# Kernel tuning notes

Hardware: AMD Instinct MI355X
Metric: run time of the kernel (lower is better)

Reference implementation:

```python
import jax, jax.numpy as jnp
import numpy as np

T = 20        # obs_len + pred_len
G = 1024      # number of scenes (groups)
P = 64        # pedestrians per scene (uniform groups)
THR = 0.25    # collision_threshold


def setup_inputs() -> dict:
    key = jax.random.key(0)
    k1, k2 = jax.random.split(key)
    trajectory = jax.random.normal(k1, (T, G * P, 2), dtype=jnp.float32)
    trajectory_relative = jax.random.normal(k2, (T, G * P, 2), dtype=jnp.float32)
    starts = jnp.arange(G, dtype=jnp.int32) * P
    seq_start_end = jnp.stack([starts, starts + P], axis=1)  # (G, 2)
    return {
        "trajectory": trajectory,
        "trajectory_relative": trajectory_relative,
        "seq_start_end": seq_start_end,
    }


def reference(trajectory, trajectory_relative, seq_start_end):
    # trajectory: (T, B, 2) with B = G*P, groups are contiguous slabs of size P
    # (uniform groups -> the ragged python loop collapses to one reshape).
    x = trajectory.transpose(1, 0, 2)            # (B, T, 2)
    x = x.reshape(G, P, T, 2).transpose(0, 2, 1, 3)  # (G, T, P, 2)

    # pairwise differences within each group at every timestep
    diff = x[:, :, :, None, :] - x[:, :, None, :, :]     # (G, T, P, P, 2)
    sq = jnp.sum(diff * diff, axis=-1)                    # (G, T, P, P)
    eye = jnp.eye(P, dtype=sq.dtype)
    # add identity under the sqrt: keeps sqrt away from 0 on the diagonal;
    # diagonal cost is 0 either way (relu(THR - d - THR*I) with d=0 or d=1).
    dist = jnp.sqrt(sq + eye)                             # (G, T, P, P)

    cost = jax.nn.relu(THR - dist - THR * eye)            # (G, T, P, P)
    # per group: (T, P*P) -> (P*P, T); concat over groups; flatten
    out = cost.reshape(G, T, P * P).transpose(0, 2, 1).reshape(-1)
    return out
```

## Files before the change

### kernel.cpp

```cpp
#include <hip/hip_runtime.h>

#define TT 20
#define GG 1024
#define PP 64
#define THR 0.25f
#define XPAD 65

#define BARRIER_LDS() asm volatile("s_waitcnt lgkmcnt(0)\n\ts_barrier" ::: "memory")

__global__ __launch_bounds__(256) void traj_critic_kernel(
    const float* __restrict__ traj, float* __restrict__ out)
{
    __shared__ float2 xs[TT * XPAD];
    __shared__ float4 buf[1280];

    const int blk  = blockIdx.x;
    const int g    = blk >> 1;
    const int half = blk & 1;
    const int tid  = threadIdx.x;

    {
        const float4* tg = (const float4*)traj;
        for (int u4 = tid; u4 < (TT * PP * 2 / 4); u4 += 256) {
            int t = u4 >> 5;
            int r = u4 & 31;
            float4 v = tg[t * 32768 + g * 32 + r];
            xs[t * XPAD + 2 * r]     = make_float2(v.x, v.y);
            xs[t * XPAD + 2 * r + 1] = make_float2(v.z, v.w);
        }
    }
    BARRIER_LDS();

    const int j   = tid & 63;
    const int wid = tid >> 6;

    float2 xj[TT];
#pragma unroll
    for (int t = 0; t < TT; ++t) xj[t] = xs[t * XPAD + j];

#pragma unroll 1
    for (int c = 0; c < 8; ++c) {
        const int i0 = half * 32 + c * 4;
        const int i  = i0 + wid;
        const float kill = (i == j) ? 0.0f : 1.0f;

        float cst[TT];
#pragma unroll
        for (int t = 0; t < TT; ++t) {
            float2 xi = xs[t * XPAD + i];
            float dx = xi.x - xj[t].x;
            float dy = xi.y - xj[t].y;
            float d  = __builtin_amdgcn_sqrtf(dx * dx + dy * dy);
            float v  = THR - d;
            v = v > 0.0f ? v : 0.0f;
            cst[t] = v * kill;
        }

#pragma unroll
        for (int kt = 0; kt < 5; ++kt) {
            int m  = 5 * tid + kt;
            int pm = (m & ~7) | ((5 * m) & 7);
            buf[pm] = make_float4(cst[4 * kt + 0], cst[4 * kt + 1],
                                  cst[4 * kt + 2], cst[4 * kt + 3]);
        }
        BARRIER_LDS();

        float4* op = (float4*)out + ((size_t)g * 20480 + (size_t)i0 * 320);
#pragma unroll
        for (int k = 0; k < 5; ++k) {
            int m  = k * 256 + tid;
            int pm = (m & ~7) | ((5 * m) & 7);
            op[m] = buf[pm];
        }
        if (c != 7) BARRIER_LDS();
    }
}

extern "C" void kernel_launch(void* const* d_in, const int* in_sizes, int n_in,
                              void* d_out, int out_size, void* d_ws, size_t ws_size,
                              hipStream_t stream) {
    const float* traj = (const float*)d_in[0];
    float* out = (float*)d_out;
    traj_critic_kernel<<<2 * GG, 256, 0, stream>>>(traj, out);
}
```

Before: 352.1 us.

## Use per-wave LDS transpose regions and readlane broadcasts, removing block barriers

Each wave now stages and transposes only its own output row in a private slice of the LDS buffer. That removes the two block-wide barriers per chunk iteration. The xi coordinates are fetched with wave-uniform readlane from registers instead of a separate padded LDS array, so the xs array is dropped and the input staging reuses buf. A launch_bounds occupancy hint of 6 is added. The intent is to cut synchronisation stalls and LDS traffic in this store-heavy kernel, at the cost of extra readlane instructions and tighter register limits.

```diff
diff --git a/kernel.cpp b/kernel.cpp
--- a/kernel.cpp
+++ b/kernel.cpp
@@ -4,52 +4,54 @@
 #define GG 1024
 #define PP 64
 #define THR 0.25f
-#define XPAD 65
 
 #define BARRIER_LDS() asm volatile("s_waitcnt lgkmcnt(0)\n\ts_barrier" ::: "memory")
 
-__global__ __launch_bounds__(256) void traj_critic_kernel(
+__global__ __launch_bounds__(256, 6) void traj_critic_kernel(
     const float* __restrict__ traj, float* __restrict__ out)
 {
-    __shared__ float2 xs[TT * XPAD];
     __shared__ float4 buf[1280];
 
     const int blk  = blockIdx.x;
     const int g    = blk >> 1;
     const int half = blk & 1;
     const int tid  = threadIdx.x;
+    const int lane = tid & 63;
+    const int wid  = tid >> 6;
 
     {
         const float4* tg = (const float4*)traj;
-        for (int u4 = tid; u4 < (TT * PP * 2 / 4); u4 += 256) {
-            int t = u4 >> 5;
-            int r = u4 & 31;
-            float4 v = tg[t * 32768 + g * 32 + r];
-            xs[t * XPAD + 2 * r]     = make_float2(v.x, v.y);
-            xs[t * XPAD + 2 * r + 1] = make_float2(v.z, v.w);
+        for (int u = tid; u < 640; u += 256) {
+            int t = u >> 5;
+            int r = u & 31;
+            buf[u] = tg[t * 32768 + g * 32 + r];
         }
     }
     BARRIER_LDS();
 
-    const int j   = tid & 63;
-    const int wid = tid >> 6;
+    float2 xj[TT];
+    const float2* xs2 = (const float2*)buf;
+#pragma unroll
+    for (int t = 0; t < TT; ++t) xj[t] = xs2[t * 64 + lane];
+    BARRIER_LDS();
 
-    float2 xj[TT];
-#pragma unroll
-    for (int t = 0; t < TT; ++t) xj[t] = xs[t * XPAD + j];
+    const int wbase = wid * 320;
+    float4* outg4 = (float4*)out + (size_t)g * 20480;
 
 #pragma unroll 1
     for (int c = 0; c < 8; ++c) {
-        const int i0 = half * 32 + c * 4;
-        const int i  = i0 + wid;
-        const float kill = (i == j) ? 0.0f : 1.0f;
+        const int i = half * 32 + c * 4 + wid;
+        const float kill = (i == lane) ? 0.0f : 1.0f;
 
         float cst[TT];
 #pragma unroll
         for (int t = 0; t < TT; ++t) {
-            float2 xi = xs[t * XPAD + i];
-            float dx = xi.x - xj[t].x;
-            float dy = xi.y - xj[t].y;
+            float xix = __int_as_float(
+                __builtin_amdgcn_readlane(__float_as_int(xj[t].x), i));
+            float xiy = __int_as_float(
+                __builtin_amdgcn_readlane(__float_as_int(xj[t].y), i));
+            float dx = xix - xj[t].x;
+            float dy = xiy - xj[t].y;
             float d  = __builtin_amdgcn_sqrtf(dx * dx + dy * dy);
             float v  = THR - d;
             v = v > 0.0f ? v : 0.0f;
@@ -58,21 +60,19 @@
 
 #pragma unroll
         for (int kt = 0; kt < 5; ++kt) {
-            int m  = 5 * tid + kt;
+            int m  = wbase + 5 * lane + kt;
             int pm = (m & ~7) | ((5 * m) & 7);
             buf[pm] = make_float4(cst[4 * kt + 0], cst[4 * kt + 1],
                                   cst[4 * kt + 2], cst[4 * kt + 3]);
         }
-        BARRIER_LDS();
 
-        float4* op = (float4*)out + ((size_t)g * 20480 + (size_t)i0 * 320);
+        float4* op = outg4 + (size_t)i * 320;
 #pragma unroll
         for (int k = 0; k < 5; ++k) {
-            int m  = k * 256 + tid;
+            int m  = wbase + k * 64 + lane;
             int pm = (m & ~7) | ((5 * m) & 7);
-            op[m] = buf[pm];
+            op[k * 64 + lane] = buf[pm];
         }
-        if (c != 7) BARRIER_LDS();
     }
 }
 
```

Result: no change. 352.2 us (+0.0%).
